# Performance work log

Hardware: AMD Instinct MI355X
Metric: run time of the kernel (lower is better)

The kernel has to match this reference:

```python
import jax, jax.numpy as jnp
import numpy as np

HEADS = 8
DIM_HEAD = 64
DIM = 512
INNER = HEADS * DIM_HEAD  # 512
SCALE = DIM_HEAD ** -0.5


def setup_inputs() -> dict:
    key = jax.random.key(0)
    k1, k2, k3, k4 = jax.random.split(key, 4)
    B, N = 2, 4096
    x = jax.random.normal(k1, (B, N, DIM), dtype=jnp.float32)
    # nn.Linear(dim, inner*3, bias=False): weight [3*inner, dim]; y = x @ W.T
    w_qkv = jax.random.normal(k2, (3 * INNER, DIM), dtype=jnp.float32) * (DIM ** -0.5)
    w_out = jax.random.normal(k3, (DIM, INNER), dtype=jnp.float32) * (INNER ** -0.5)
    b_out = jax.random.normal(k4, (DIM,), dtype=jnp.float32) * 0.01
    return {"x": x, "w_qkv": w_qkv, "w_out": w_out, "b_out": b_out, "H": 64, "W": 64}


def reference(x, w_qkv, w_out, b_out, H, W):
    B, N, _ = x.shape
    qkv = jnp.einsum('bnd,ed->bne', x, w_qkv)  # [B, N, 3*inner]
    q, k, v = jnp.split(qkv, 3, axis=-1)
    def to_heads(t):
        return t.reshape(B, N, HEADS, DIM_HEAD).transpose(0, 2, 1, 3)  # b h n d
    q, k, v = to_heads(q), to_heads(k), to_heads(v)
    dots = jnp.einsum('bhid,bhjd->bhij', q, k) * SCALE
    attn = jax.nn.softmax(dots, axis=-1)  # dropout p=0.0 -> identity
    out = jnp.einsum('bhij,bhjd->bhid', attn, v)
    out = out.transpose(0, 2, 1, 3).reshape(B, N, INNER)
    return jnp.einsum('bne,de->bnd', out, w_out) + b_out
```

## Files before the change

### kernel.cpp

```cpp
#include <hip/hip_runtime.h>
#include <hip/hip_bf16.h>

typedef __hip_bfloat16 bf16;
typedef __attribute__((ext_vector_type(8))) short short8;
typedef __attribute__((ext_vector_type(4))) short shortx4;
typedef __attribute__((ext_vector_type(4))) float floatx4;
typedef __attribute__((ext_vector_type(4))) int intx4;

#define MFMA16(a, b, c) __builtin_amdgcn_mfma_f32_16x16x32_bf16((a), (b), (c), 0, 0, 0)
#define EXP2(x) __builtin_amdgcn_exp2f(x)

__device__ __forceinline__ short f2s(float v) {
    return __builtin_bit_cast(short, __float2bfloat16(v));
}

__device__ __forceinline__ int packhi(float lo, float hi) {
    return (int)__builtin_amdgcn_perm(__builtin_bit_cast(unsigned, hi),
                                      __builtin_bit_cast(unsigned, lo),
                                      0x07060302u);
}

__device__ __forceinline__ short8 cvt8v(float4 f0, float4 f1) {
    short8 r;
    r[0] = f2s(f0.x); r[1] = f2s(f0.y); r[2] = f2s(f0.z); r[3] = f2s(f0.w);
    r[4] = f2s(f1.x); r[5] = f2s(f1.y); r[6] = f2s(f1.z); r[7] = f2s(f1.w);
    return r;
}

__global__ __launch_bounds__(256) void cvt_inputs(
    const float* __restrict__ x, const float* __restrict__ wq,
    const float* __restrict__ wo, bf16* __restrict__ xb,
    bf16* __restrict__ wqb, bf16* __restrict__ wob)
{
    int idx = blockIdx.x * 256 + threadIdx.x;
    const float* src;
    bf16* dst;
    int off;
    if (idx < 524288)      { src = x;  dst = xb;  off = idx; }
    else if (idx < 622592) { src = wq; dst = wqb; off = idx - 524288; }
    else                   { src = wo; dst = wob; off = idx - 622592; }
    float4 f0 = ((const float4*)src)[off * 2];
    float4 f1 = ((const float4*)src)[off * 2 + 1];
    *(short8*)&((short*)dst)[off * 8] = cvt8v(f0, f1);
}

__global__ __launch_bounds__(256) void qkv_gemm(
    const bf16* __restrict__ xb, const bf16* __restrict__ wqb,
    bf16* __restrict__ q, bf16* __restrict__ k, bf16* __restrict__ vt)
{
    __shared__ short pool[20480];
    short (*As)[128][40] = (short(*)[128][40])pool;
    short (*Bs)[128][40] = (short(*)[128][40])(pool + 10240);
    short (*Qt)[144] = (short(*)[144])pool;
    short (*Vt)[136] = (short(*)[136])pool;
    const int t = threadIdx.x;
    const int bm = blockIdx.x * 128;
    const int be = blockIdx.y * 128;
    const int w = t >> 6, lane = t & 63, lq = lane >> 4, lm = lane & 15;
    const int wr = w >> 1, wc = w & 1;
    const int srow = t >> 1, scol = (t & 1) * 16;
    const float C = 0.18033688011112042f;

    const bf16* xp = &xb[(size_t)(bm + srow) * 512 + scol];
    const bf16* wp = &wqb[(size_t)(be + srow) * 512 + scol];

    intx4 xr[2], wr4[2];
    auto issue = [&](int k0) {
        xr[0] = *(const intx4*)(xp + k0);
        xr[1] = *(const intx4*)(xp + k0 + 8);
        wr4[0] = *(const intx4*)(wp + k0);
        wr4[1] = *(const intx4*)(wp + k0 + 8);
    };
    auto commit = [&](int buf) {
        *(intx4*)&As[buf][srow][scol]     = xr[0];
        *(intx4*)&As[buf][srow][scol + 8] = xr[1];
        *(intx4*)&Bs[buf][srow][scol]     = wr4[0];
        *(intx4*)&Bs[buf][srow][scol + 8] = wr4[1];
    };

    floatx4 acc[4][4];
#pragma unroll
    for (int i = 0; i < 4; ++i)
#pragma unroll
        for (int j = 0; j < 4; ++j) acc[i][j] = {0.f, 0.f, 0.f, 0.f};

    issue(0);
    commit(0);
    __syncthreads();
    int cur = 0;
    for (int k0 = 0; k0 < 512; k0 += 32) {
        const bool more = (k0 + 32) < 512;
        if (more) issue(k0 + 32);
        short8 af[4], bf[4];
#pragma unroll
        for (int mt = 0; mt < 4; ++mt) af[mt] = *(const short8*)&As[cur][wr * 64 + mt * 16 + lm][lq * 8];
#pragma unroll
        for (int nt = 0; nt < 4; ++nt) bf[nt] = *(const short8*)&Bs[cur][wc * 64 + nt * 16 + lm][lq * 8];
#pragma unroll
        for (int mt = 0; mt < 4; ++mt)
#pragma unroll
            for (int nt = 0; nt < 4; ++nt)
                acc[mt][nt] = MFMA16(af[mt], bf[nt], acc[mt][nt]);
        if (more) {
            commit(cur ^ 1);
            __syncthreads();
        }
        cur ^= 1;
    }

    const int which = be >> 9;
    __syncthreads();
    if (which < 2) {
        const float scale = (which == 0) ? C : 1.0f;
#pragma unroll
        for (int nt = 0; nt < 4; ++nt) {
            const int e_loc = wc * 64 + nt * 16 + lm;
#pragma unroll
            for (int mt = 0; mt < 4; ++mt)
#pragma unroll
                for (int r = 0; r < 4; ++r)
                    Qt[wr * 64 + mt * 16 + lq * 4 + r][e_loc] = f2s(acc[mt][nt][r] * scale);
        }
        __syncthreads();
        bf16* dst = (which == 0) ? q : k;
        const int tr = t >> 1, th = t & 1;
        const int grow = bm + tr;
        const int b = grow >> 12, n = grow & 4095;
        const int h = ((be + th * 64) & 511) >> 6;
        bf16* p = dst + ((size_t)(b * 8 + h) * 4096 + n) * 64;
#pragma unroll
        for (int c = 0; c < 8; ++c)
            *(intx4*)&p[c * 8] = *(const intx4*)&Qt[tr][th * 64 + c * 8];
    } else {
#pragma unroll
        for (int nt = 0; nt < 4; ++nt) {
            const int e_loc = wc * 64 + nt * 16 + lm;
#pragma unroll
            for (int mt = 0; mt < 4; ++mt) {
                const int col = wr * 64 + 4 * (mt & 1) + 8 * lq + 32 * (mt >> 1);
                shortx4 v4;
#pragma unroll
                for (int r = 0; r < 4; ++r) v4[r] = f2s(acc[mt][nt][r]);
                *(shortx4*)&Vt[e_loc][col] = v4;
            }
        }
        __syncthreads();
        const int b = bm >> 12, n0 = bm & 4095;
        const int h0 = (be - 1024) >> 6;
        const int row = t >> 1, cb = (t & 1) * 64;
        const int h = h0 + (row >> 6), d = row & 63;
        const size_t gb = ((size_t)(b * 8 + h) * 64 + d) * 4096 + n0 + cb;
#pragma unroll
        for (int c = 0; c < 8; ++c)
            *(intx4*)&vt[gb + c * 8] = *(const intx4*)&Vt[row][cb + c * 8];
    }
}

__global__ __launch_bounds__(256, 2) void flash_attn(
    const bf16* __restrict__ q, const bf16* __restrict__ k,
    const bf16* __restrict__ vt, bf16* __restrict__ out)
{
    __shared__ short Qs[128][72];
    __shared__ short Ks[2][64][72];
    __shared__ short Vs[2][64][72];
    const int t = threadIdx.x;
    const int i0 = blockIdx.x * 128;
    const int bh = blockIdx.y;
    const int w = t >> 6, lane = t & 63, lq = lane >> 4, lm = lane & 15;
    const floatx4 zero4 = {0.f, 0.f, 0.f, 0.f};

    const size_t nbase = (size_t)bh * 4096 * 64;
    const size_t vbase = (size_t)bh * 64 * 4096;
    const int r0 = t >> 3, c0 = (t & 7) * 8;

#pragma unroll
    for (int it = 0; it < 4; ++it) {
        int off = it * 2048 + t * 8;
        int row = off >> 6, col = off & 63;
        *(intx4*)&Qs[row][col] = *(const intx4*)&q[nbase + (size_t)(i0 + row) * 64 + col];
    }

    intx4 kreg[2], vreg[2];
    auto issue = [&](int j0n) {
        kreg[0] = *(const intx4*)&k[nbase + (size_t)(j0n + r0) * 64 + c0];
        kreg[1] = *(const intx4*)&k[nbase + (size_t)(j0n + 32 + r0) * 64 + c0];
        vreg[0] = *(const intx4*)&vt[vbase + (size_t)r0 * 4096 + j0n + c0];
        vreg[1] = *(const intx4*)&vt[vbase + (size_t)(32 + r0) * 4096 + j0n + c0];
    };
    auto commit = [&](int buf) {
        *(intx4*)&Ks[buf][r0][c0]      = kreg[0];
        *(intx4*)&Ks[buf][32 + r0][c0] = kreg[1];
        *(intx4*)&Vs[buf][r0][c0]      = vreg[0];
        *(intx4*)&Vs[buf][32 + r0][c0] = vreg[1];
    };

    issue(0);
    commit(0);
    __syncthreads();
    short8 aq0[2], aq1[2];
#pragma unroll
    for (int g = 0; g < 2; ++g) {
        aq0[g] = *(const short8*)&Qs[g * 64 + w * 16 + lm][lq * 8];
        aq1[g] = *(const short8*)&Qs[g * 64 + w * 16 + lm][32 + lq * 8];
    }

    float l_lane[2] = {0.f, 0.f};
    floatx4 o_acc[2][4];
#pragma unroll
    for (int g = 0; g < 2; ++g)
#pragma unroll
        for (int dt = 0; dt < 4; ++dt) o_acc[g][dt] = zero4;

    int cur = 0;
    for (int j0 = 0; j0 < 4096; j0 += 64) {
        const bool more = (j0 + 64) < 4096;
        if (more) issue(j0 + 64);

        floatx4 s[2][4];
#pragma unroll
        for (int jt = 0; jt < 4; ++jt) {
            short8 bk0 = *(const short8*)&Ks[cur][jt * 16 + lm][lq * 8];
            short8 bk1 = *(const short8*)&Ks[cur][jt * 16 + lm][32 + lq * 8];
#pragma unroll
            for (int g = 0; g < 2; ++g) {
                s[g][jt] = MFMA16(bk0, aq0[g], zero4);
                s[g][jt] = MFMA16(bk1, aq1[g], s[g][jt]);
            }
        }

        short8 bp0[2], bp1[2];
#pragma unroll
        for (int g = 0; g < 2; ++g) {
            intx4 pkA, pkB;
#pragma unroll
            for (int jt = 0; jt < 4; ++jt) {
                float e0 = EXP2(s[g][jt][0]);
                float e1 = EXP2(s[g][jt][1]);
                float e2 = EXP2(s[g][jt][2]);
                float e3 = EXP2(s[g][jt][3]);
                l_lane[g] += (e0 + e1) + (e2 + e3);
                if (jt < 2) {
                    pkA[jt * 2]     = packhi(e0, e1);
                    pkA[jt * 2 + 1] = packhi(e2, e3);
                } else {
                    pkB[(jt - 2) * 2]     = packhi(e0, e1);
                    pkB[(jt - 2) * 2 + 1] = packhi(e2, e3);
                }
            }
            bp0[g] = __builtin_bit_cast(short8, pkA);
            bp1[g] = __builtin_bit_cast(short8, pkB);
        }

#pragma unroll
        for (int dt = 0; dt < 4; ++dt) {
            short8 av0 = *(const short8*)&Vs[cur][dt * 16 + lm][lq * 8];
            short8 av1 = *(const short8*)&Vs[cur][dt * 16 + lm][32 + lq * 8];
#pragma unroll
            for (int g = 0; g < 2; ++g) {
                o_acc[g][dt] = MFMA16(av0, bp0[g], o_acc[g][dt]);
                o_acc[g][dt] = MFMA16(av1, bp1[g], o_acc[g][dt]);
            }
        }

        if (more) {
            commit(cur ^ 1);
            __syncthreads();
        }
        cur ^= 1;
    }

    const int b = bh >> 3, h = bh & 7;
    short* Os = (short*)Qs;
    const int obase = w * 1024;
    const int il = lane >> 2, c = (lane & 3) * 16;
#pragma unroll
    for (int g = 0; g < 2; ++g) {
        float l = l_lane[g];
        l += __shfl_xor(l, 16);
        l += __shfl_xor(l, 32);
        const float inv_l = 1.0f / l;
        __syncthreads();
#pragma unroll
        for (int dt = 0; dt < 4; ++dt)
#pragma unroll
            for (int r = 0; r < 4; ++r)
                Os[obase + lm * 64 + dt * 16 + lq * 4 + r] = f2s(o_acc[g][dt][r] * inv_l);
        __syncthreads();
        const int i = i0 + g * 64 + w * 16 + il;
        intx4 v0 = *(const intx4*)&Os[obase + il * 64 + c];
        intx4 v1 = *(const intx4*)&Os[obase + il * 64 + c + 8];
        *(intx4*)&out[((size_t)b * 4096 + i) * 512 + h * 64 + c] = v0;
        *(intx4*)&out[((size_t)b * 4096 + i) * 512 + h * 64 + c + 8] = v1;
    }
}

__global__ __launch_bounds__(256) void out_gemm(
    const bf16* __restrict__ a, const bf16* __restrict__ wob,
    const float* __restrict__ bias, float* __restrict__ y)
{
    __shared__ short As[2][128][40];
    __shared__ short Bs[2][64][40];
    const int t = threadIdx.x;
    const int bm = blockIdx.x * 128;
    const int be = blockIdx.y * 64;
    const int w = t >> 6, lane = t & 63, lq = lane >> 4, lm = lane & 15;
    const int wr = w >> 1, wc = w & 1;
    const int srow = t >> 1, scol = (t & 1) * 16;
    const int brow = t >> 2, bcol = (t & 3) * 8;

    const bf16* ap = &a[(size_t)(bm + srow) * 512 + scol];
    const bf16* wp = &wob[(size_t)(be + brow) * 512 + bcol];

    intx4 ar[2], br;
    auto issue = [&](int k0) {
        ar[0] = *(const intx4*)(ap + k0);
        ar[1] = *(const intx4*)(ap + k0 + 8);
        br    = *(const intx4*)(wp + k0);
    };
    auto commit = [&](int buf) {
        *(intx4*)&As[buf][srow][scol]     = ar[0];
        *(intx4*)&As[buf][srow][scol + 8] = ar[1];
        *(intx4*)&Bs[buf][brow][bcol]     = br;
    };

    floatx4 acc[4][2];
#pragma unroll
    for (int i = 0; i < 4; ++i)
#pragma unroll
        for (int j = 0; j < 2; ++j) acc[i][j] = {0.f, 0.f, 0.f, 0.f};

    issue(0);
    commit(0);
    __syncthreads();
    int cur = 0;
    for (int k0 = 0; k0 < 512; k0 += 32) {
        const bool more = (k0 + 32) < 512;
        if (more) issue(k0 + 32);
        short8 af[4], bf[2];
#pragma unroll
        for (int mt = 0; mt < 4; ++mt) af[mt] = *(const short8*)&As[cur][wr * 64 + mt * 16 + lm][lq * 8];
#pragma unroll
        for (int nt = 0; nt < 2; ++nt) bf[nt] = *(const short8*)&Bs[cur][wc * 32 + nt * 16 + lm][lq * 8];
#pragma unroll
        for (int mt = 0; mt < 4; ++mt)
#pragma unroll
            for (int nt = 0; nt < 2; ++nt)
                acc[mt][nt] = MFMA16(af[mt], bf[nt], acc[mt][nt]);
        if (more) {
            commit(cur ^ 1);
            __syncthreads();
        }
        cur ^= 1;
    }

#pragma unroll
    for (int nt = 0; nt < 2; ++nt) {
        const int gcol = be + wc * 32 + nt * 16 + lm;
        const float bv = bias[gcol];
#pragma unroll
        for (int mt = 0; mt < 4; ++mt) {
#pragma unroll
            for (int r = 0; r < 4; ++r) {
                int grow = bm + wr * 64 + mt * 16 + lq * 4 + r;
                y[(size_t)grow * 512 + gcol] = acc[mt][nt][r] + bv;
            }
        }
    }
}

extern "C" void kernel_launch(void* const* d_in, const int* in_sizes, int n_in,
                              void* d_out, int out_size, void* d_ws, size_t ws_size,
                              hipStream_t stream) {
    const float* x     = (const float*)d_in[0];
    const float* w_qkv = (const float*)d_in[1];
    const float* w_out = (const float*)d_in[2];
    const float* b_out = (const float*)d_in[3];

    const size_t HEAD_ELEMS = (size_t)16 * 4096 * 64;
    bf16* qw  = (bf16*)d_ws;
    bf16* kw  = qw + HEAD_ELEMS;
    bf16* vtw = kw + HEAD_ELEMS;
    bf16* aw  = vtw + HEAD_ELEMS;
    bf16* xb  = aw + HEAD_ELEMS;
    bf16* wqb = xb + (size_t)8192 * 512;
    bf16* wob = wqb + (size_t)1536 * 512;
    float* y  = (float*)d_out;

    cvt_inputs<<<2560, 256, 0, stream>>>(x, w_qkv, w_out, xb, wqb, wob);
    qkv_gemm<<<dim3(64, 12), 256, 0, stream>>>(xb, wqb, qw, kw, vtw);
    flash_attn<<<dim3(32, 16), 256, 0, stream>>>(qw, kw, vtw, aw);
    out_gemm<<<dim3(64, 8), 256, 0, stream>>>(aw, wob, b_out, y);
}
```

Baseline: 192.3 us.

## Enlarge flash-attention query tile to 256 rows with swizzled LDS

Each flash_attn block now handles 256 query rows, each wave 64, instead of 128. That doubles how often each K/V tile is reused, and the launch becomes a 1-D grid of 256 blocks with an interleaved block-to-(head, tile) mapping. Padded shared-memory arrays are replaced by an XOR-swizzled layout to avoid bank conflicts without padding. The exp/pack step is fused right after each QK MFMA pair, and the epilogue drops the block-wide barriers because each wave writes only its own region. The cost is more accumulator registers and only one block (4 waves) per CU, which reduces latency hiding.

Measured after the change: 214.8 us. 1.12x slower.

```diff
diff --git a/kernel.cpp b/kernel.cpp
--- a/kernel.cpp
+++ b/kernel.cpp
@@ -25,6 +25,10 @@
     r[0] = f2s(f0.x); r[1] = f2s(f0.y); r[2] = f2s(f0.z); r[3] = f2s(f0.w);
     r[4] = f2s(f1.x); r[5] = f2s(f1.y); r[6] = f2s(f1.z); r[7] = f2s(f1.w);
     return r;
+}
+
+__device__ __forceinline__ int swz(int row, int chunk) {
+    return row * 64 + ((chunk ^ (row & 7)) << 3);
 }
 
 __global__ __launch_bounds__(256) void cvt_inputs(
@@ -156,58 +160,62 @@
     }
 }
 
-__global__ __launch_bounds__(256, 2) void flash_attn(
+__global__ __launch_bounds__(256, 1) void flash_attn(
     const bf16* __restrict__ q, const bf16* __restrict__ k,
     const bf16* __restrict__ vt, bf16* __restrict__ out)
 {
-    __shared__ short Qs[128][72];
-    __shared__ short Ks[2][64][72];
-    __shared__ short Vs[2][64][72];
+    __shared__ short Qs[16384];
+    __shared__ short Ks[2][4096];
+    __shared__ short Vs[2][4096];
     const int t = threadIdx.x;
-    const int i0 = blockIdx.x * 128;
-    const int bh = blockIdx.y;
+    const int n = blockIdx.x;
+    const int L = (n & 7) * 32 + (n >> 3);
+    const int i0 = (L & 15) * 256;
+    const int bh = L >> 4;
     const int w = t >> 6, lane = t & 63, lq = lane >> 4, lm = lane & 15;
     const floatx4 zero4 = {0.f, 0.f, 0.f, 0.f};
 
     const size_t nbase = (size_t)bh * 4096 * 64;
     const size_t vbase = (size_t)bh * 64 * 4096;
-    const int r0 = t >> 3, c0 = (t & 7) * 8;
-
-#pragma unroll
-    for (int it = 0; it < 4; ++it) {
-        int off = it * 2048 + t * 8;
-        int row = off >> 6, col = off & 63;
-        *(intx4*)&Qs[row][col] = *(const intx4*)&q[nbase + (size_t)(i0 + row) * 64 + col];
+    const int r0 = t >> 3, ch = t & 7;
+
+#pragma unroll
+    for (int it = 0; it < 8; ++it) {
+        int row = it * 32 + r0;
+        *(intx4*)&Qs[swz(row, ch)] =
+            *(const intx4*)&q[nbase + (size_t)(i0 + row) * 64 + ch * 8];
     }
 
     intx4 kreg[2], vreg[2];
     auto issue = [&](int j0n) {
-        kreg[0] = *(const intx4*)&k[nbase + (size_t)(j0n + r0) * 64 + c0];
-        kreg[1] = *(const intx4*)&k[nbase + (size_t)(j0n + 32 + r0) * 64 + c0];
-        vreg[0] = *(const intx4*)&vt[vbase + (size_t)r0 * 4096 + j0n + c0];
-        vreg[1] = *(const intx4*)&vt[vbase + (size_t)(32 + r0) * 4096 + j0n + c0];
+        kreg[0] = *(const intx4*)&k[nbase + (size_t)(j0n + r0) * 64 + ch * 8];
+        kreg[1] = *(const intx4*)&k[nbase + (size_t)(j0n + 32 + r0) * 64 + ch * 8];
+        vreg[0] = *(const intx4*)&vt[vbase + (size_t)r0 * 4096 + j0n + ch * 8];
+        vreg[1] = *(const intx4*)&vt[vbase + (size_t)(32 + r0) * 4096 + j0n + ch * 8];
     };
     auto commit = [&](int buf) {
-        *(intx4*)&Ks[buf][r0][c0]      = kreg[0];
-        *(intx4*)&Ks[buf][32 + r0][c0] = kreg[1];
-        *(intx4*)&Vs[buf][r0][c0]      = vreg[0];
-        *(intx4*)&Vs[buf][32 + r0][c0] = vreg[1];
+        *(intx4*)&Ks[buf][swz(r0, ch)]      = kreg[0];
+        *(intx4*)&Ks[buf][swz(32 + r0, ch)] = kreg[1];
+        *(intx4*)&Vs[buf][swz(r0, ch)]      = vreg[0];
+        *(intx4*)&Vs[buf][swz(32 + r0, ch)] = vreg[1];
     };
 
     issue(0);
     commit(0);
     __syncthreads();
-    short8 aq0[2], aq1[2];
-#pragma unroll
-    for (int g = 0; g < 2; ++g) {
-        aq0[g] = *(const short8*)&Qs[g * 64 + w * 16 + lm][lq * 8];
-        aq1[g] = *(const short8*)&Qs[g * 64 + w * 16 + lm][32 + lq * 8];
-    }
-
-    float l_lane[2] = {0.f, 0.f};
-    floatx4 o_acc[2][4];
-#pragma unroll
-    for (int g = 0; g < 2; ++g)
+
+    short8 aq0[4], aq1[4];
+#pragma unroll
+    for (int g = 0; g < 4; ++g) {
+        const int qrow = w * 64 + g * 16 + lm;
+        aq0[g] = *(const short8*)&Qs[swz(qrow, lq)];
+        aq1[g] = *(const short8*)&Qs[swz(qrow, 4 + lq)];
+    }
+
+    float l_lane[4] = {0.f, 0.f, 0.f, 0.f};
+    floatx4 o_acc[4][4];
+#pragma unroll
+    for (int g = 0; g < 4; ++g)
 #pragma unroll
         for (int dt = 0; dt < 4; ++dt) o_acc[g][dt] = zero4;
 
@@ -216,49 +224,36 @@
         const bool more = (j0 + 64) < 4096;
         if (more) issue(j0 + 64);
 
-        floatx4 s[2][4];
+        intx4 pka[4], pkb[4];
 #pragma unroll
         for (int jt = 0; jt < 4; ++jt) {
-            short8 bk0 = *(const short8*)&Ks[cur][jt * 16 + lm][lq * 8];
-            short8 bk1 = *(const short8*)&Ks[cur][jt * 16 + lm][32 + lq * 8];
-#pragma unroll
-            for (int g = 0; g < 2; ++g) {
-                s[g][jt] = MFMA16(bk0, aq0[g], zero4);
-                s[g][jt] = MFMA16(bk1, aq1[g], s[g][jt]);
+            const int krow = jt * 16 + lm;
+            short8 bk0 = *(const short8*)&Ks[cur][swz(krow, lq)];
+            short8 bk1 = *(const short8*)&Ks[cur][swz(krow, 4 + lq)];
+#pragma unroll
+            for (int g = 0; g < 4; ++g) {
+                floatx4 s4 = MFMA16(bk0, aq0[g], zero4);
+                s4 = MFMA16(bk1, aq1[g], s4);
+                float e0 = EXP2(s4[0]);
+                float e1 = EXP2(s4[1]);
+                float e2 = EXP2(s4[2]);
+                float e3 = EXP2(s4[3]);
+                l_lane[g] += (e0 + e1) + (e2 + e3);
+                int p01 = packhi(e0, e1), p23 = packhi(e2, e3);
+                if (jt < 2) { pka[g][jt * 2] = p01; pka[g][jt * 2 + 1] = p23; }
+                else        { pkb[g][(jt - 2) * 2] = p01; pkb[g][(jt - 2) * 2 + 1] = p23; }
             }
         }
 
-        short8 bp0[2], bp1[2];
-#pragma unroll
-        for (int g = 0; g < 2; ++g) {
-            intx4 pkA, pkB;
-#pragma unroll
-            for (int jt = 0; jt < 4; ++jt) {
-                float e0 = EXP2(s[g][jt][0]);
-                float e1 = EXP2(s[g][jt][1]);
-                float e2 = EXP2(s[g][jt][2]);
-                float e3 = EXP2(s[g][jt][3]);
-                l_lane[g] += (e0 + e1) + (e2 + e3);
-                if (jt < 2) {
-                    pkA[jt * 2]     = packhi(e0, e1);
-                    pkA[jt * 2 + 1] = packhi(e2, e3);
-                } else {
-                    pkB[(jt - 2) * 2]     = packhi(e0, e1);
-                    pkB[(jt - 2) * 2 + 1] = packhi(e2, e3);
-                }
-            }
-            bp0[g] = __builtin_bit_cast(short8, pkA);
-            bp1[g] = __builtin_bit_cast(short8, pkB);
-        }
-
 #pragma unroll
         for (int dt = 0; dt < 4; ++dt) {
-            short8 av0 = *(const short8*)&Vs[cur][dt * 16 + lm][lq * 8];
-            short8 av1 = *(const short8*)&Vs[cur][dt * 16 + lm][32 + lq * 8];
-#pragma unroll
-            for (int g = 0; g < 2; ++g) {
-                o_acc[g][dt] = MFMA16(av0, bp0[g], o_acc[g][dt]);
-                o_acc[g][dt] = MFMA16(av1, bp1[g], o_acc[g][dt]);
+            const int vrow = dt * 16 + lm;
+            short8 av0 = *(const short8*)&Vs[cur][swz(vrow, lq)];
+            short8 av1 = *(const short8*)&Vs[cur][swz(vrow, 4 + lq)];
+#pragma unroll
+            for (int g = 0; g < 4; ++g) {
+                o_acc[g][dt] = MFMA16(av0, __builtin_bit_cast(short8, pka[g]), o_acc[g][dt]);
+                o_acc[g][dt] = MFMA16(av1, __builtin_bit_cast(short8, pkb[g]), o_acc[g][dt]);
             }
         }
 
@@ -270,27 +265,25 @@
     }
 
     const int b = bh >> 3, h = bh & 7;
-    short* Os = (short*)Qs;
+    short* Os = Qs;
     const int obase = w * 1024;
-    const int il = lane >> 2, c = (lane & 3) * 16;
-#pragma unroll
-    for (int g = 0; g < 2; ++g) {
+    const int il = lane >> 2, cc = (lane & 3) * 16;
+#pragma unroll
+    for (int g = 0; g < 4; ++g) {
         float l = l_lane[g];
         l += __shfl_xor(l, 16);
         l += __shfl_xor(l, 32);
         const float inv_l = 1.0f / l;
-        __syncthreads();
 #pragma unroll
         for (int dt = 0; dt < 4; ++dt)
 #pragma unroll
             for (int r = 0; r < 4; ++r)
                 Os[obase + lm * 64 + dt * 16 + lq * 4 + r] = f2s(o_acc[g][dt][r] * inv_l);
-        __syncthreads();
-        const int i = i0 + g * 64 + w * 16 + il;
-        intx4 v0 = *(const intx4*)&Os[obase + il * 64 + c];
-        intx4 v1 = *(const intx4*)&Os[obase + il * 64 + c + 8];
-        *(intx4*)&out[((size_t)b * 4096 + i) * 512 + h * 64 + c] = v0;
-        *(intx4*)&out[((size_t)b * 4096 + i) * 512 + h * 64 + c + 8] = v1;
+        const int i = i0 + w * 64 + g * 16 + il;
+        intx4 v0 = *(const intx4*)&Os[obase + il * 64 + cc];
+        intx4 v1 = *(const intx4*)&Os[obase + il * 64 + cc + 8];
+        *(intx4*)&out[((size_t)b * 4096 + i) * 512 + h * 64 + cc] = v0;
+        *(intx4*)&out[((size_t)b * 4096 + i) * 512 + h * 64 + cc + 8] = v1;
     }
 }
 
@@ -388,6 +381,6 @@
 
     cvt_inputs<<<2560, 256, 0, stream>>>(x, w_qkv, w_out, xb, wqb, wob);
     qkv_gemm<<<dim3(64, 12), 256, 0, stream>>>(xb, wqb, qw, kw, vtw);
-    flash_attn<<<dim3(32, 16), 256, 0, stream>>>(qw, kw, vtw, aw);
+    flash_attn<<<dim3(256), 256, 0, stream>>>(qw, kw, vtw, aw);
     out_gemm<<<dim3(64, 8), 256, 0, stream>>>(aw, wob, b_out, y);
 }
```
